# Optimization experiments

Hardware: AMD Instinct MI355X
Metric: run time of the kernel (lower is better)

## Reference

```python
import jax, jax.numpy as jnp
import numpy as np

N_NODES = 50000


def _gcn_conv(x, src, dst, W, b, n):
    # linear transform first (PyG GCNConv: self.lin has no bias; bias added after aggregation)
    h = x @ W  # [N, out]
    # symmetric normalization with self-loops already appended in (src, dst)
    ones = jnp.ones(src.shape[0], dtype=h.dtype)
    deg = jax.ops.segment_sum(ones, dst, num_segments=n)  # in-degree incl. self-loop
    dinv = jnp.where(deg > 0, jax.lax.rsqrt(deg), 0.0)
    norm = dinv[src] * dinv[dst]  # [E+N]
    msg = h[src] * norm[:, None]  # gather + scale
    out = jax.ops.segment_sum(msg, dst, num_segments=n)  # scatter-add
    return out + b


def setup_inputs() -> dict:
    key = jax.random.key(0)
    ks = jax.random.split(key, 8)
    f_in, h1, h2, n_cls = 256, 128, 128, 40
    E = 800000
    x = jax.random.normal(ks[0], (N_NODES, f_in), dtype=jnp.float32)
    edge_index = jax.random.randint(ks[1], (2, E), 0, N_NODES, dtype=jnp.int64)
    def glorot(k, fi, fo):
        s = jnp.sqrt(6.0 / (fi + fo)).astype(jnp.float32)
        return jax.random.uniform(k, (fi, fo), jnp.float32, -s, s)
    return {
        "x": x,
        "edge_index": edge_index,
        "W1": glorot(ks[2], f_in, h1), "b1": jnp.zeros((h1,), jnp.float32),
        "W2": glorot(ks[3], h1, h2), "b2": jnp.zeros((h2,), jnp.float32),
        "W3": glorot(ks[4], h2, n_cls), "b3": jnp.zeros((n_cls,), jnp.float32),
    }


def reference(x, edge_index, W1, b1, W2, b2, W3, b3):
    n = x.shape[0]
    loop = jnp.arange(n, dtype=edge_index.dtype)
    src = jnp.concatenate([edge_index[0], loop])  # add self-loops (fill_value=1.0)
    dst = jnp.concatenate([edge_index[1], loop])
    h = _gcn_conv(x, src, dst, W1, b1, n)
    h = jax.nn.relu(h)  # dropout is identity in eval mode
    h = _gcn_conv(h, src, dst, W2, b2, n)
    h = jax.nn.relu(h)
    h = _gcn_conv(h, src, dst, W3, b3, n)
    return jax.nn.log_softmax(h, axis=1)
```

## Files before the change

### kernel.cpp

```cpp
#include <hip/hip_runtime.h>
#include <cstdint>
#include <cstddef>
#include <cmath>


typedef __attribute__((ext_vector_type(8))) short short8;
typedef __attribute__((ext_vector_type(4))) float f32x4;

constexpr int EPB = 4096;

__device__ __forceinline__ ushort f2bf(float f) {
  union { float f; uint32_t u; } x; x.f = f;
  uint32_t r = x.u + 0x7fffu + ((x.u >> 16) & 1u);
  return (ushort)(r >> 16);
}
__device__ __forceinline__ float bf2f(ushort u) {
  union { uint32_t u; float f; } x; x.u = ((uint32_t)u) << 16;
  return x.f;
}

__global__ __launch_bounds__(256) void bucket_hist_kernel(const int* __restrict__ dst,
                                                          int* __restrict__ bucket_count,
                                                          int E) {
  __shared__ int h[256];
  const int t  = threadIdx.x;
  const int e0 = blockIdx.x * EPB;
  const int myE = min(EPB, E - e0);
  h[t] = 0;
  __syncthreads();
  for (int i = t; i < myE; i += 256) atomicAdd(&h[dst[e0 + i] >> 8], 1);
  __syncthreads();
  if (h[t]) atomicAdd(&bucket_count[t], h[t]);
}

__global__ __launch_bounds__(256) void bucket_scan_kernel(const int* __restrict__ bucket_count,
                                                          int* __restrict__ bucket_offs,
                                                          int* __restrict__ bucket_cursor,
                                                          int* __restrict__ offs,
                                                          int nbuck, int n) {
  __shared__ int s[256];
  const int t = threadIdx.x;
  const int c = (t < nbuck) ? bucket_count[t] : 0;
  s[t] = c;
  __syncthreads();
  for (int off = 1; off < 256; off <<= 1) {
    int v = (t >= off) ? s[t - off] : 0;
    __syncthreads();
    s[t] += v;
    __syncthreads();
  }
  if (t < nbuck) {
    bucket_offs[t]   = s[t] - c;
    bucket_cursor[t] = s[t] - c;
  }
  if (t == 255) {
    bucket_offs[nbuck] = s[255];
    offs[n] = s[255];
  }
}

__global__ __launch_bounds__(256) void bucket_scatter_kernel(const int* __restrict__ src,
                                                             const int* __restrict__ dst,
                                                             int* __restrict__ bucket_cursor,
                                                             uint32_t* __restrict__ staged,
                                                             int E, int nbuck) {
  __shared__ int hist[256], s[256], lstart[256], cbase[256], lcur[256];
  __shared__ uint32_t stage[EPB];
  const int t  = threadIdx.x;
  const int e0 = blockIdx.x * EPB;
  const int myE = min(EPB, E - e0);
  hist[t] = 0;
  __syncthreads();
  for (int i = t; i < myE; i += 256) atomicAdd(&hist[dst[e0 + i] >> 8], 1);
  __syncthreads();
  const int c = hist[t];
  s[t] = c;
  __syncthreads();
  for (int off = 1; off < 256; off <<= 1) {
    int v = (t >= off) ? s[t - off] : 0;
    __syncthreads();
    s[t] += v;
    __syncthreads();
  }
  lstart[t] = s[t] - c;
  lcur[t]   = s[t] - c;
  cbase[t]  = (c > 0 && t < nbuck) ? atomicAdd(&bucket_cursor[t], c) : 0;
  __syncthreads();
  for (int i = t; i < myE; i += 256) {
    const int sv = src[e0 + i], dv = dst[e0 + i];
    const int slot = atomicAdd(&lcur[dv >> 8], 1);
    stage[slot] = (uint32_t)sv | ((uint32_t)dv << 16);
  }
  __syncthreads();
  for (int i = t; i < myE; i += 256) {
    const uint32_t sd = stage[i];
    const int b = sd >> 24;
    staged[cbase[b] + (i - lstart[b])] = sd;
  }
}

__global__ __launch_bounds__(256) void bucket_csr_kernel(const uint32_t* __restrict__ staged,
                                                         const int* __restrict__ bucket_offs,
                                                         int* __restrict__ offs,
                                                         float* __restrict__ dinv, int n) {
  __shared__ int cnt[256], s[256];
  const int t = threadIdx.x, b = blockIdx.x;
  cnt[t] = 0;
  __syncthreads();
  const int ebeg = bucket_offs[b], eend = bucket_offs[b + 1];
  for (int i = ebeg + t; i < eend; i += 256) atomicAdd(&cnt[(staged[i] >> 16) & 255], 1);
  __syncthreads();
  const int c = cnt[t];
  s[t] = c;
  __syncthreads();
  for (int off = 1; off < 256; off <<= 1) {
    int v = (t >= off) ? s[t - off] : 0;
    __syncthreads();
    s[t] += v;
    __syncthreads();
  }
  const int node = (b << 8) + t;
  if (node < n) {
    offs[node] = ebeg + s[t] - c;
    dinv[node] = rsqrtf((float)(c + 1));
  }
}

__global__ __launch_bounds__(256) void bucket_fill_kernel(const uint32_t* __restrict__ staged,
                                                          const int* __restrict__ bucket_offs,
                                                          const float* __restrict__ dinv,
                                                          uint32_t* __restrict__ epk, int n) {
  __shared__ int cnt[256], s[256], cur[256];
  const int t = threadIdx.x, b = blockIdx.x;
  cnt[t] = 0;
  __syncthreads();
  const int ebeg = bucket_offs[b], eend = bucket_offs[b + 1];
  for (int i = ebeg + t; i < eend; i += 256) atomicAdd(&cnt[(staged[i] >> 16) & 255], 1);
  __syncthreads();
  const int c = cnt[t];
  s[t] = c;
  __syncthreads();
  for (int off = 1; off < 256; off <<= 1) {
    int v = (t >= off) ? s[t - off] : 0;
    __syncthreads();
    s[t] += v;
    __syncthreads();
  }
  cur[t] = ebeg + s[t] - c;
  __syncthreads();
  for (int i = ebeg + t; i < eend; i += 256) {
    const uint32_t sd = staged[i];
    const int sv = sd & 0xFFFF;
    const int dv = sd >> 16;
    const int pos = atomicAdd(&cur[dv & 255], 1);
    epk[pos] = (uint32_t)sv | ((uint32_t)f2bf(dinv[sv] * dinv[dv]) << 16);
  }
}

__global__ __launch_bounds__(256) void pack_w_kernel(const float* __restrict__ W,
                                                     ushort* __restrict__ Wp,
                                                     int K, int N, int NF) {
  const int idx  = blockIdx.x * blockDim.x + threadIdx.x;
  const int lane = idx & 63;
  const int nf   = (idx >> 6) % NF;
  const int g    = idx / (64 * NF);
  if (g * 32 >= K) return;
  const int n  = nf * 16 + (lane & 15);
  const int kb = g * 32 + (lane >> 4) * 8;
  ushort v[8];
#pragma unroll
  for (int j = 0; j < 8; ++j) {
    const float f = (n < N) ? W[(size_t)(kb + j) * N + n] : 0.f;
    v[j] = f2bf(f);
  }
  *(short8*)&Wp[((size_t)(g * NF + nf) * 64 + lane) * 8] = *(short8*)v;
}

template <int NF>
__global__ __launch_bounds__(256) void mfma_gemm_kernel(const float* __restrict__ A,
                                                        const ushort* __restrict__ Wp,
                                                        ushort* __restrict__ C,
                                                        int M, int N, int K) {
  __shared__ ushort Atile[64 * 64];
  const int tid  = threadIdx.x;
  const int lane = tid & 63;
  const int wave = tid >> 6;
  const int brow = blockIdx.x * 64;

  f32x4 acc[NF];
#pragma unroll
  for (int nf = 0; nf < NF; ++nf) acc[nf] = (f32x4){0.f, 0.f, 0.f, 0.f};

  const int arow = wave * 16 + (lane & 15);
  const int ahi  = lane >> 4;
  const int row0 = tid >> 3;
  const int kc0  = tid & 7;

  for (int k0 = 0; k0 < K; k0 += 64) {
    if (k0) __syncthreads();
#pragma unroll
    for (int c = 0; c < 2; ++c) {
      const int row = row0 + c * 32;
      const int gr  = brow + row;
      short8 v = (short8){0, 0, 0, 0, 0, 0, 0, 0};
      if (gr < M) {
        const float* Ap = A + (size_t)gr * K + k0 + kc0 * 8;
        const float4 f0 = *(const float4*)Ap;
        const float4 f1 = *(const float4*)(Ap + 4);
        v[0] = (short)f2bf(f0.x); v[1] = (short)f2bf(f0.y);
        v[2] = (short)f2bf(f0.z); v[3] = (short)f2bf(f0.w);
        v[4] = (short)f2bf(f1.x); v[5] = (short)f2bf(f1.y);
        v[6] = (short)f2bf(f1.z); v[7] = (short)f2bf(f1.w);
      }
      *(short8*)&Atile[row * 64 + ((kc0 ^ (row & 7)) * 8)] = v;
    }
    __syncthreads();

    const int gbase = (k0 >> 5) * NF;
#pragma unroll
    for (int kk = 0; kk < 2; ++kk) {
      const int kc = kk * 4 + ahi;
      const short8 a =
          *(const short8*)&Atile[arow * 64 + ((kc ^ (arow & 7)) * 8)];
      const ushort* wp = Wp + ((size_t)(gbase + kk * NF) * 64 + lane) * 8;
#pragma unroll
      for (int nf = 0; nf < NF; ++nf) {
        const short8 b = *(const short8*)(wp + (size_t)nf * 64 * 8);
        acc[nf] = __builtin_amdgcn_mfma_f32_16x16x32_bf16(a, b, acc[nf], 0, 0, 0);
      }
    }
  }

  const int crow0 = brow + wave * 16 + (lane >> 4) * 4;
  const int ccol  = lane & 15;
#pragma unroll
  for (int nf = 0; nf < NF; ++nf) {
    const int col = nf * 16 + ccol;
    if (col < N) {
#pragma unroll
      for (int r = 0; r < 4; ++r) {
        const int row = crow0 + r;
        if (row < M) C[(size_t)row * N + col] = f2bf(acc[nf][r]);
      }
    }
  }
}

template <int NF, bool BIAS_RELU_AGG, bool LSM>
__global__ __launch_bounds__(1024) void fused_agg_gemm_kernel(
    const ushort* __restrict__ h, const int* __restrict__ offsets,
    const uint32_t* __restrict__ epk, const float* __restrict__ dinv,
    const float* __restrict__ bias_agg, const ushort* __restrict__ Wp,
    const float* __restrict__ bias_out, void* __restrict__ Cv, int M, int N) {
  __shared__ ushort Atile[2][16 * 64];
  __shared__ float  Lg[16][40];
  const int tid  = threadIdx.x;
  const int lane = tid & 63;
  const int wave = tid >> 6;
  const int brow = blockIdx.x * 16;
  const int node = brow + wave;

  const int eg    = lane >> 4;
  const int l15   = lane & 15;
  const int f0    = l15 * 8;
  const int ktile = l15 >> 3;
  const int kca   = l15 & 7;

  float a8[8];
#pragma unroll
  for (int j = 0; j < 8; ++j) a8[j] = 0.f;
  if (node < M) {
    const int start = offsets[node];
    const int end   = offsets[node + 1];
    for (int eb = start; eb < end; eb += 8) {
      const int e0 = eb + eg;
      const int e1 = e0 + 4;
      if (e0 < end) {
        const uint32_t p0 = epk[e0];
        const float    w0 = bf2f((ushort)(p0 >> 16));
        const short8   hv0 = *(const short8*)&h[(size_t)(p0 & 0xFFFF) * 128 + f0];
        if (e1 < end) {
          const uint32_t p1 = epk[e1];
          const float    w1 = bf2f((ushort)(p1 >> 16));
          const short8   hv1 = *(const short8*)&h[(size_t)(p1 & 0xFFFF) * 128 + f0];
#pragma unroll
          for (int j = 0; j < 8; ++j) {
            a8[j] = fmaf(bf2f((ushort)hv0[j]), w0, a8[j]);
            a8[j] = fmaf(bf2f((ushort)hv1[j]), w1, a8[j]);
          }
        } else {
#pragma unroll
          for (int j = 0; j < 8; ++j) a8[j] = fmaf(bf2f((ushort)hv0[j]), w0, a8[j]);
        }
      }
    }
#pragma unroll
    for (int j = 0; j < 8; ++j) {
      a8[j] += __shfl_xor(a8[j], 16, 64);
      a8[j] += __shfl_xor(a8[j], 32, 64);
    }
  }
  if (eg == 0) {
    ushort o[8];
    if (node < M) {
      const float di  = dinv[node];
      const float di2 = di * di;
      const short8 hs = *(const short8*)&h[(size_t)node * 128 + f0];
#pragma unroll
      for (int j = 0; j < 8; ++j) {
        float a = fmaf(bf2f((ushort)hs[j]), di2, a8[j]);
        if (BIAS_RELU_AGG) a = fmaxf(a + bias_agg[f0 + j], 0.f);
        o[j] = f2bf(a);
      }
    } else {
#pragma unroll
      for (int j = 0; j < 8; ++j) o[j] = 0;
    }
    *(short8*)&Atile[ktile][wave * 64 + ((kca ^ (wave & 7)) << 3)] = *(short8*)o;
  }
  __syncthreads();

  if (wave < NF) {
    const int nf = wave;
    f32x4 acc = (f32x4){0.f, 0.f, 0.f, 0.f};
    const int arow = lane & 15;
    const int ahi  = lane >> 4;
#pragma unroll
    for (int kt = 0; kt < 2; ++kt) {
#pragma unroll
      for (int kk = 0; kk < 2; ++kk) {
        const int kc = kk * 4 + ahi;
        const short8 a =
            *(const short8*)&Atile[kt][arow * 64 + ((kc ^ (arow & 7)) * 8)];
        const int g = kt * 2 + kk;
        const short8 b = *(const short8*)(Wp + ((size_t)(g * NF + nf) * 64 + lane) * 8);
        acc = __builtin_amdgcn_mfma_f32_16x16x32_bf16(a, b, acc, 0, 0, 0);
      }
    }
    const int ccol = lane & 15;
    const int r0   = (lane >> 4) * 4;
    const int col  = nf * 16 + ccol;
    if constexpr (!LSM) {
      ushort* C = (ushort*)Cv;
      if (col < N) {
#pragma unroll
        for (int r = 0; r < 4; ++r) {
          const int row = brow + r0 + r;
          if (row < M) C[(size_t)row * N + col] = f2bf(acc[r]);
        }
      }
    } else {
      if (col < N) {
        const float bv = bias_out[col];
#pragma unroll
        for (int r = 0; r < 4; ++r) Lg[r0 + r][col] = acc[r] + bv;
      }
    }
  }
  if constexpr (LSM) {
    __syncthreads();
    if (wave == 0) {
      float* out = (float*)Cv;
      const bool act = lane < N;
      for (int r = 0; r < 16; ++r) {
        const int row = brow + r;
        float v = act ? Lg[r][lane] : -INFINITY;
        float m = v;
#pragma unroll
        for (int o = 32; o >= 1; o >>= 1) m = fmaxf(m, __shfl_xor(m, o, 64));
        float ex = act ? expf(v - m) : 0.f;
        float s = ex;
#pragma unroll
        for (int o = 32; o >= 1; o >>= 1) s += __shfl_xor(s, o, 64);
        if (act && row < M) out[(size_t)row * N + lane] = v - m - logf(s);
      }
    }
  }
}

template <bool BIAS_RELU>
__global__ __launch_bounds__(256) void agg4_kernel(const ushort* __restrict__ h,
                                                   const int* __restrict__ offsets,
                                                   const uint32_t* __restrict__ epk,
                                                   const float* __restrict__ dinv,
                                                   const float* __restrict__ bias,
                                                   ushort* __restrict__ out, int n) {
  const int wave = threadIdx.x >> 6;
  const int lane = threadIdx.x & 63;
  const int node = blockIdx.x * 4 + wave;
  if (node >= n) return;
  const int eg = lane >> 4;
  const int f0 = (lane & 15) * 8;

  float acc[8];
#pragma unroll
  for (int j = 0; j < 8; ++j) acc[j] = 0.f;

  const int start = offsets[node];
  const int end   = offsets[node + 1];
  for (int eb = start; eb < end; eb += 8) {
    const int e0 = eb + eg;
    const int e1 = e0 + 4;
    if (e0 < end) {
      const uint32_t p0 = epk[e0];
      const float    w0 = bf2f((ushort)(p0 >> 16));
      const short8   hv0 = *(const short8*)&h[(size_t)(p0 & 0xFFFF) * 128 + f0];
      if (e1 < end) {
        const uint32_t p1 = epk[e1];
        const float    w1 = bf2f((ushort)(p1 >> 16));
        const short8   hv1 = *(const short8*)&h[(size_t)(p1 & 0xFFFF) * 128 + f0];
#pragma unroll
        for (int j = 0; j < 8; ++j) {
          acc[j] = fmaf(bf2f((ushort)hv0[j]), w0, acc[j]);
          acc[j] = fmaf(bf2f((ushort)hv1[j]), w1, acc[j]);
        }
      } else {
#pragma unroll
        for (int j = 0; j < 8; ++j) acc[j] = fmaf(bf2f((ushort)hv0[j]), w0, acc[j]);
      }
    }
  }
#pragma unroll
  for (int j = 0; j < 8; ++j) {
    acc[j] += __shfl_xor(acc[j], 16, 64);
    acc[j] += __shfl_xor(acc[j], 32, 64);
  }
  if (eg == 0) {
    const float di  = dinv[node];
    const float di2 = di * di;
    const short8 hs = *(const short8*)&h[(size_t)node * 128 + f0];
    ushort o[8];
#pragma unroll
    for (int j = 0; j < 8; ++j) {
      float a = fmaf(bf2f((ushort)hs[j]), di2, acc[j]);
      if (BIAS_RELU) a = fmaxf(a + bias[f0 + j], 0.f);
      o[j] = f2bf(a);
    }
    *(short8*)&out[(size_t)node * 128 + f0] = *(short8*)o;
  }
}

extern "C" void kernel_launch(void* const* d_in, const int* in_sizes, int n_in,
                              void* d_out, int out_size, void* d_ws, size_t ws_size,
                              hipStream_t stream) {
  const float* x  = (const float*)d_in[0];
  const int*   ei = (const int*)d_in[1];
  const float* W1 = (const float*)d_in[2];
  const float* b1 = (const float*)d_in[3];
  const float* W2 = (const float*)d_in[4];
  const float* b2 = (const float*)d_in[5];
  const float* W3 = (const float*)d_in[6];
  const float* b3 = (const float*)d_in[7];

  const int h1   = in_sizes[3];
  const int h2   = in_sizes[5];
  const int ncls = in_sizes[7];
  const int fin  = in_sizes[2] / h1;
  const int n    = in_sizes[0] / fin;
  const int E    = in_sizes[1] / 2;

  const int* src = ei;
  const int* dst = ei + E;

  char* p = (char*)d_ws;
  auto alloc = [&](size_t bytes) {
    char* r = p;
    p += (bytes + 255) & ~size_t(255);
    return r;
  };
  float*    dinv   = (float*)alloc((size_t)n * 4);
  int*      offs   = (int*)alloc((size_t)(n + 1) * 4);
  int*      bcount = (int*)alloc(256 * 4);
  int*      boffs  = (int*)alloc(257 * 4);
  int*      bcur   = (int*)alloc(256 * 4);
  uint32_t* staged = (uint32_t*)alloc((size_t)E * 4);
  uint32_t* epk    = (uint32_t*)alloc((size_t)E * 4);
  ushort*   hf     = (ushort*)alloc((size_t)n * h1 * 2);
  ushort*   hg     = (ushort*)alloc((size_t)n * h1 * 2);
  ushort*   Wp1    = (ushort*)alloc((size_t)(fin / 32) * 8 * 64 * 8 * 2);
  ushort*   Wp2    = (ushort*)alloc((size_t)(h1 / 32) * 8 * 64 * 8 * 2);
  ushort*   Wp3    = (ushort*)alloc((size_t)(h2 / 32) * 3 * 64 * 8 * 2);

  const int nbuck = (n + 255) >> 8;
  const int ebw   = (E + EPB - 1) / EPB;

  hipMemsetAsync(bcount, 0, 256 * 4, stream);
  bucket_hist_kernel<<<ebw, 256, 0, stream>>>(dst, bcount, E);
  bucket_scan_kernel<<<1, 256, 0, stream>>>(bcount, boffs, bcur, offs, nbuck, n);
  bucket_scatter_kernel<<<ebw, 256, 0, stream>>>(src, dst, bcur, staged, E, nbuck);
  bucket_csr_kernel<<<nbuck, 256, 0, stream>>>(staged, boffs, offs, dinv, n);
  bucket_fill_kernel<<<nbuck, 256, 0, stream>>>(staged, boffs, dinv, epk, n);

  {
    int t1 = (fin / 32) * 8 * 64;
    int t2 = (h1 / 32) * 8 * 64;
    int t3 = (h2 / 32) * 3 * 64;
    pack_w_kernel<<<(t1 + 255) / 256, 256, 0, stream>>>(W1, Wp1, fin, h1, 8);
    pack_w_kernel<<<(t2 + 255) / 256, 256, 0, stream>>>(W2, Wp2, h1, h2, 8);
    pack_w_kernel<<<(t3 + 255) / 256, 256, 0, stream>>>(W3, Wp3, h2, ncls, 3);
  }

  const int gblocks = (n + 63) / 64;
  const int ablocks = (n + 3) / 4;
  const int fblocks = (n + 15) / 16;

  mfma_gemm_kernel<8><<<gblocks, 256, 0, stream>>>(x, Wp1, hf, n, h1, fin);
  fused_agg_gemm_kernel<8, true, false><<<fblocks, 1024, 0, stream>>>(
      hf, offs, epk, dinv, b1, Wp2, nullptr, hg, n, h2);
  agg4_kernel<true><<<ablocks, 256, 0, stream>>>(hg, offs, epk, dinv, b2, hf, n);
  fused_agg_gemm_kernel<3, false, true><<<fblocks, 1024, 0, stream>>>(
      hf, offs, epk, dinv, nullptr, Wp3, b3, d_out, n, ncls);
}
```

Baseline: 237.7 us.

## Unfuse aggregation from GEMM and transform before aggregating in layer three

```diff
diff --git a/kernel.cpp b/kernel.cpp
--- a/kernel.cpp
+++ b/kernel.cpp
@@ -5,6 +5,7 @@
 
 
 typedef __attribute__((ext_vector_type(8))) short short8;
+typedef __attribute__((ext_vector_type(4))) short short4v;
 typedef __attribute__((ext_vector_type(4))) float f32x4;
 
 constexpr int EPB = 4096;
@@ -176,8 +177,8 @@
   *(short8*)&Wp[((size_t)(g * NF + nf) * 64 + lane) * 8] = *(short8*)v;
 }
 
-template <int NF>
-__global__ __launch_bounds__(256) void mfma_gemm_kernel(const float* __restrict__ A,
+template <int NF, bool AF32>
+__global__ __launch_bounds__(256) void mfma_gemm_kernel(const void* __restrict__ Av,
                                                         const ushort* __restrict__ Wp,
                                                         ushort* __restrict__ C,
                                                         int M, int N, int K) {
@@ -204,13 +205,17 @@
       const int gr  = brow + row;
       short8 v = (short8){0, 0, 0, 0, 0, 0, 0, 0};
       if (gr < M) {
-        const float* Ap = A + (size_t)gr * K + k0 + kc0 * 8;
-        const float4 f0 = *(const float4*)Ap;
-        const float4 f1 = *(const float4*)(Ap + 4);
-        v[0] = (short)f2bf(f0.x); v[1] = (short)f2bf(f0.y);
-        v[2] = (short)f2bf(f0.z); v[3] = (short)f2bf(f0.w);
-        v[4] = (short)f2bf(f1.x); v[5] = (short)f2bf(f1.y);
-        v[6] = (short)f2bf(f1.z); v[7] = (short)f2bf(f1.w);
+        if constexpr (AF32) {
+          const float* A = (const float*)Av + (size_t)gr * K + k0 + kc0 * 8;
+          const float4 f0 = *(const float4*)A;
+          const float4 f1 = *(const float4*)(A + 4);
+          v[0] = (short)f2bf(f0.x); v[1] = (short)f2bf(f0.y);
+          v[2] = (short)f2bf(f0.z); v[3] = (short)f2bf(f0.w);
+          v[4] = (short)f2bf(f1.x); v[5] = (short)f2bf(f1.y);
+          v[6] = (short)f2bf(f1.z); v[7] = (short)f2bf(f1.w);
+        } else {
+          v = *(const short8*)((const ushort*)Av + (size_t)gr * K + k0 + kc0 * 8);
+        }
       }
       *(short8*)&Atile[row * 64 + ((kc0 ^ (row & 7)) * 8)] = v;
     }
@@ -236,144 +241,10 @@
 #pragma unroll
   for (int nf = 0; nf < NF; ++nf) {
     const int col = nf * 16 + ccol;
-    if (col < N) {
-#pragma unroll
-      for (int r = 0; r < 4; ++r) {
-        const int row = crow0 + r;
-        if (row < M) C[(size_t)row * N + col] = f2bf(acc[nf][r]);
-      }
-    }
-  }
-}
-
-template <int NF, bool BIAS_RELU_AGG, bool LSM>
-__global__ __launch_bounds__(1024) void fused_agg_gemm_kernel(
-    const ushort* __restrict__ h, const int* __restrict__ offsets,
-    const uint32_t* __restrict__ epk, const float* __restrict__ dinv,
-    const float* __restrict__ bias_agg, const ushort* __restrict__ Wp,
-    const float* __restrict__ bias_out, void* __restrict__ Cv, int M, int N) {
-  __shared__ ushort Atile[2][16 * 64];
-  __shared__ float  Lg[16][40];
-  const int tid  = threadIdx.x;
-  const int lane = tid & 63;
-  const int wave = tid >> 6;
-  const int brow = blockIdx.x * 16;
-  const int node = brow + wave;
-
-  const int eg    = lane >> 4;
-  const int l15   = lane & 15;
-  const int f0    = l15 * 8;
-  const int ktile = l15 >> 3;
-  const int kca   = l15 & 7;
-
-  float a8[8];
-#pragma unroll
-  for (int j = 0; j < 8; ++j) a8[j] = 0.f;
-  if (node < M) {
-    const int start = offsets[node];
-    const int end   = offsets[node + 1];
-    for (int eb = start; eb < end; eb += 8) {
-      const int e0 = eb + eg;
-      const int e1 = e0 + 4;
-      if (e0 < end) {
-        const uint32_t p0 = epk[e0];
-        const float    w0 = bf2f((ushort)(p0 >> 16));
-        const short8   hv0 = *(const short8*)&h[(size_t)(p0 & 0xFFFF) * 128 + f0];
-        if (e1 < end) {
-          const uint32_t p1 = epk[e1];
-          const float    w1 = bf2f((ushort)(p1 >> 16));
-          const short8   hv1 = *(const short8*)&h[(size_t)(p1 & 0xFFFF) * 128 + f0];
-#pragma unroll
-          for (int j = 0; j < 8; ++j) {
-            a8[j] = fmaf(bf2f((ushort)hv0[j]), w0, a8[j]);
-            a8[j] = fmaf(bf2f((ushort)hv1[j]), w1, a8[j]);
-          }
-        } else {
-#pragma unroll
-          for (int j = 0; j < 8; ++j) a8[j] = fmaf(bf2f((ushort)hv0[j]), w0, a8[j]);
-        }
-      }
-    }
-#pragma unroll
-    for (int j = 0; j < 8; ++j) {
-      a8[j] += __shfl_xor(a8[j], 16, 64);
-      a8[j] += __shfl_xor(a8[j], 32, 64);
-    }
-  }
-  if (eg == 0) {
-    ushort o[8];
-    if (node < M) {
-      const float di  = dinv[node];
-      const float di2 = di * di;
-      const short8 hs = *(const short8*)&h[(size_t)node * 128 + f0];
-#pragma unroll
-      for (int j = 0; j < 8; ++j) {
-        float a = fmaf(bf2f((ushort)hs[j]), di2, a8[j]);
-        if (BIAS_RELU_AGG) a = fmaxf(a + bias_agg[f0 + j], 0.f);
-        o[j] = f2bf(a);
-      }
-    } else {
-#pragma unroll
-      for (int j = 0; j < 8; ++j) o[j] = 0;
-    }
-    *(short8*)&Atile[ktile][wave * 64 + ((kca ^ (wave & 7)) << 3)] = *(short8*)o;
-  }
-  __syncthreads();
-
-  if (wave < NF) {
-    const int nf = wave;
-    f32x4 acc = (f32x4){0.f, 0.f, 0.f, 0.f};
-    const int arow = lane & 15;
-    const int ahi  = lane >> 4;
-#pragma unroll
-    for (int kt = 0; kt < 2; ++kt) {
-#pragma unroll
-      for (int kk = 0; kk < 2; ++kk) {
-        const int kc = kk * 4 + ahi;
-        const short8 a =
-            *(const short8*)&Atile[kt][arow * 64 + ((kc ^ (arow & 7)) * 8)];
-        const int g = kt * 2 + kk;
-        const short8 b = *(const short8*)(Wp + ((size_t)(g * NF + nf) * 64 + lane) * 8);
-        acc = __builtin_amdgcn_mfma_f32_16x16x32_bf16(a, b, acc, 0, 0, 0);
-      }
-    }
-    const int ccol = lane & 15;
-    const int r0   = (lane >> 4) * 4;
-    const int col  = nf * 16 + ccol;
-    if constexpr (!LSM) {
-      ushort* C = (ushort*)Cv;
-      if (col < N) {
-#pragma unroll
-        for (int r = 0; r < 4; ++r) {
-          const int row = brow + r0 + r;
-          if (row < M) C[(size_t)row * N + col] = f2bf(acc[r]);
-        }
-      }
-    } else {
-      if (col < N) {
-        const float bv = bias_out[col];
-#pragma unroll
-        for (int r = 0; r < 4; ++r) Lg[r0 + r][col] = acc[r] + bv;
-      }
-    }
-  }
-  if constexpr (LSM) {
-    __syncthreads();
-    if (wave == 0) {
-      float* out = (float*)Cv;
-      const bool act = lane < N;
-      for (int r = 0; r < 16; ++r) {
-        const int row = brow + r;
-        float v = act ? Lg[r][lane] : -INFINITY;
-        float m = v;
-#pragma unroll
-        for (int o = 32; o >= 1; o >>= 1) m = fmaxf(m, __shfl_xor(m, o, 64));
-        float ex = act ? expf(v - m) : 0.f;
-        float s = ex;
-#pragma unroll
-        for (int o = 32; o >= 1; o >>= 1) s += __shfl_xor(s, o, 64);
-        if (act && row < M) out[(size_t)row * N + lane] = v - m - logf(s);
-      }
+#pragma unroll
+    for (int r = 0; r < 4; ++r) {
+      const int row = crow0 + r;
+      if (row < M) C[(size_t)row * N + col] = f2bf(acc[nf][r]);
     }
   }
 }
@@ -440,6 +311,78 @@
   }
 }
 
+__global__ __launch_bounds__(256) void agg40_lsm_kernel(const ushort* __restrict__ h,
+                                                        const int* __restrict__ offsets,
+                                                        const uint32_t* __restrict__ epk,
+                                                        const float* __restrict__ dinv,
+                                                        const float* __restrict__ bias,
+                                                        float* __restrict__ out, int n) {
+  const int wave = threadIdx.x >> 6;
+  const int lane = threadIdx.x & 63;
+  const int node = blockIdx.x * 4 + wave;
+  if (node >= n) return;
+  const int eg  = lane >> 4;
+  const int l15 = lane & 15;
+  const int f0  = l15 * 4;
+
+  float acc[4] = {0.f, 0.f, 0.f, 0.f};
+  const int start = offsets[node];
+  const int end   = offsets[node + 1];
+  for (int eb = start; eb < end; eb += 8) {
+    const int e0 = eb + eg;
+    const int e1 = e0 + 4;
+    if (e0 < end) {
+      const uint32_t p0 = epk[e0];
+      const float    w0 = bf2f((ushort)(p0 >> 16));
+      const short4v  hv0 = *(const short4v*)&h[(size_t)(p0 & 0xFFFF) * 64 + f0];
+      if (e1 < end) {
+        const uint32_t p1 = epk[e1];
+        const float    w1 = bf2f((ushort)(p1 >> 16));
+        const short4v  hv1 = *(const short4v*)&h[(size_t)(p1 & 0xFFFF) * 64 + f0];
+#pragma unroll
+        for (int j = 0; j < 4; ++j) {
+          acc[j] = fmaf(bf2f((ushort)hv0[j]), w0, acc[j]);
+          acc[j] = fmaf(bf2f((ushort)hv1[j]), w1, acc[j]);
+        }
+      } else {
+#pragma unroll
+        for (int j = 0; j < 4; ++j) acc[j] = fmaf(bf2f((ushort)hv0[j]), w0, acc[j]);
+      }
+    }
+  }
+#pragma unroll
+  for (int j = 0; j < 4; ++j) {
+    acc[j] += __shfl_xor(acc[j], 16, 64);
+    acc[j] += __shfl_xor(acc[j], 32, 64);
+  }
+  if (eg == 0) {
+    const bool valid = l15 < 10;
+    const float di  = dinv[node];
+    const float di2 = di * di;
+    const short4v hs = *(const short4v*)&h[(size_t)node * 64 + f0];
+    float v[4];
+    if (valid) {
+#pragma unroll
+      for (int j = 0; j < 4; ++j)
+        v[j] = fmaf(bf2f((ushort)hs[j]), di2, acc[j]) + bias[f0 + j];
+    } else {
+#pragma unroll
+      for (int j = 0; j < 4; ++j) v[j] = -INFINITY;
+    }
+    float m = fmaxf(fmaxf(v[0], v[1]), fmaxf(v[2], v[3]));
+#pragma unroll
+    for (int o = 8; o >= 1; o >>= 1) m = fmaxf(m, __shfl_xor(m, o, 64));
+    float s = valid ? (expf(v[0] - m) + expf(v[1] - m) + expf(v[2] - m) + expf(v[3] - m)) : 0.f;
+#pragma unroll
+    for (int o = 8; o >= 1; o >>= 1) s += __shfl_xor(s, o, 64);
+    const float mls = m + logf(s);
+    if (valid) {
+      float4 o4 = make_float4(v[0] - mls, v[1] - mls, v[2] - mls, v[3] - mls);
+      *(float4*)&out[(size_t)node * 40 + f0] = o4;
+    }
+  }
+}
+
 extern "C" void kernel_launch(void* const* d_in, const int* in_sizes, int n_in,
                               void* d_out, int out_size, void* d_ws, size_t ws_size,
                               hipStream_t stream) {
@@ -475,11 +418,12 @@
   int*      bcur   = (int*)alloc(256 * 4);
   uint32_t* staged = (uint32_t*)alloc((size_t)E * 4);
   uint32_t* epk    = (uint32_t*)alloc((size_t)E * 4);
-  ushort*   hf     = (ushort*)alloc((size_t)n * h1 * 2);
-  ushort*   hg     = (ushort*)alloc((size_t)n * h1 * 2);
+  ushort*   bufA   = (ushort*)alloc((size_t)n * h1 * 2);
+  ushort*   bufB   = (ushort*)alloc((size_t)n * h1 * 2);
+  ushort*   hs     = (ushort*)alloc((size_t)n * 64 * 2);
   ushort*   Wp1    = (ushort*)alloc((size_t)(fin / 32) * 8 * 64 * 8 * 2);
   ushort*   Wp2    = (ushort*)alloc((size_t)(h1 / 32) * 8 * 64 * 8 * 2);
-  ushort*   Wp3    = (ushort*)alloc((size_t)(h2 / 32) * 3 * 64 * 8 * 2);
+  ushort*   Wp3    = (ushort*)alloc((size_t)(h2 / 32) * 4 * 64 * 8 * 2);
 
   const int nbuck = (n + 255) >> 8;
   const int ebw   = (E + EPB - 1) / EPB;
@@ -494,20 +438,20 @@
   {
     int t1 = (fin / 32) * 8 * 64;
     int t2 = (h1 / 32) * 8 * 64;
-    int t3 = (h2 / 32) * 3 * 64;
+    int t3 = (h2 / 32) * 4 * 64;
     pack_w_kernel<<<(t1 + 255) / 256, 256, 0, stream>>>(W1, Wp1, fin, h1, 8);
     pack_w_kernel<<<(t2 + 255) / 256, 256, 0, stream>>>(W2, Wp2, h1, h2, 8);
-    pack_w_kernel<<<(t3 + 255) / 256, 256, 0, stream>>>(W3, Wp3, h2, ncls, 3);
+    pack_w_kernel<<<(t3 + 255) / 256, 256, 0, stream>>>(W3, Wp3, h2, ncls, 4);
   }
 
   const int gblocks = (n + 63) / 64;
   const int ablocks = (n + 3) / 4;
-  const int fblocks = (n + 15) / 16;
-
-  mfma_gemm_kernel<8><<<gblocks, 256, 0, stream>>>(x, Wp1, hf, n, h1, fin);
-  fused_agg_gemm_kernel<8, true, false><<<fblocks, 1024, 0, stream>>>(
-      hf, offs, epk, dinv, b1, Wp2, nullptr, hg, n, h2);
-  agg4_kernel<true><<<ablocks, 256, 0, stream>>>(hg, offs, epk, dinv, b2, hf, n);
-  fused_agg_gemm_kernel<3, false, true><<<fblocks, 1024, 0, stream>>>(
-      hf, offs, epk, dinv, nullptr, Wp3, b3, d_out, n, ncls);
-}
+
+  mfma_gemm_kernel<8, true><<<gblocks, 256, 0, stream>>>(x, Wp1, bufA, n, h1, fin);
+  agg4_kernel<true><<<ablocks, 256, 0, stream>>>(bufA, offs, epk, dinv, b1, bufB, n);
+  mfma_gemm_kernel<8, false><<<gblocks, 256, 0, stream>>>(bufB, Wp2, bufA, n, h2, h1);
+  agg4_kernel<true><<<ablocks, 256, 0, stream>>>(bufA, offs, epk, dinv, b2, bufB, n);
+  mfma_gemm_kernel<4, false><<<gblocks, 256, 0, stream>>>(bufB, Wp3, hs, n, 64, h2);
+  agg40_lsm_kernel<<<ablocks, 256, 0, stream>>>(hs, offs, epk, dinv, b3,
+                                                (float*)d_out, n);
+}
```

New measurement: 207.7 us. 1.14x faster.
